# Kernel tuning notes

Hardware: AMD Instinct MI355X
Metric: run time of the kernel (lower is better)

## Reference

```python
import jax, jax.numpy as jnp
import numpy as np

NUM_GRAPHS = 512

def setup_inputs() -> dict:
    key = jax.random.key(0)
    ks = jax.random.split(key, 6)
    N, E, D = 100000, 1600000, 128
    x = jax.random.normal(ks[0], (N, D), dtype=jnp.float32)
    edge_index = jax.random.randint(ks[1], (2, E), 0, N, dtype=jnp.int64)
    batch = jnp.sort(jax.random.randint(ks[2], (N,), 0, NUM_GRAPHS, dtype=jnp.int64))
    scale = 1.0 / np.sqrt(D)
    Ws = jax.random.normal(ks[3], (4, D, D), dtype=jnp.float32) * scale
    bs = jnp.zeros((4, D), dtype=jnp.float32)
    Wl = jax.random.normal(ks[4], (D, 1), dtype=jnp.float32) * scale
    bl = jnp.zeros((1,), dtype=jnp.float32)
    return {"x": x, "edge_index": edge_index, "batch": batch,
            "Ws": Ws, "bs": bs, "Wl": Wl, "bl": bl}

def reference(x, edge_index, batch, Ws, bs, Wl, bl):
    N = x.shape[0]
    loops = jnp.arange(N, dtype=edge_index.dtype)
    # GCNConv: add self-loops, symmetric normalization D^{-1/2} A D^{-1/2}
    row = jnp.concatenate([edge_index[0], loops])  # source nodes
    col = jnp.concatenate([edge_index[1], loops])  # target nodes
    deg = jax.ops.segment_sum(jnp.ones_like(col, dtype=x.dtype), col, num_segments=N)
    dinv = jnp.where(deg > 0, jax.lax.rsqrt(jnp.maximum(deg, 1.0)), 0.0)
    norm = dinv[row] * dinv[col]  # [E+N]
    h = x
    for i in range(Ws.shape[0]):
        h = h @ Ws[i]                                   # [N, D]
        msg = h[row] * norm[:, None]                    # gather + scale, [E+N, D]
        h = jax.ops.segment_sum(msg, col, num_segments=N) + bs[i]
        h = jax.nn.relu(h)                              # dropout is identity in eval
    # global_mean_pool over graphs
    sums = jax.ops.segment_sum(h, batch, num_segments=NUM_GRAPHS)
    cnt = jax.ops.segment_sum(jnp.ones((N,), h.dtype), batch, num_segments=NUM_GRAPHS)
    pooled = sums / jnp.maximum(cnt, 1.0)[:, None]      # [G, D]
    return pooled @ Wl + bl                             # [G, 1]
```

## Files before the change

kernel.cpp:

```cpp
#include <hip/hip_runtime.h>


constexpr int D = 128;
constexpr int NGRAPH = 512;
constexpr int CHUNK = 4096;
constexpr int BSH = 9;
constexpr int OP = 136;

typedef __attribute__((ext_vector_type(8))) short bf16x8;
typedef __attribute__((ext_vector_type(4))) float f32x4;

__device__ __forceinline__ float bf2f(unsigned short b) {
    return __uint_as_float(((unsigned int)b) << 16);
}
__device__ __forceinline__ unsigned short f2bf(float f) {
    unsigned int u = __float_as_uint(f);
    u += 0x7FFFu + ((u >> 16) & 1u);
    return (unsigned short)(u >> 16);
}

__global__ __launch_bounds__(256) void setup_all(
        const float4* __restrict__ x4, ushort4* __restrict__ hb, int n4, int CB,
        const float* __restrict__ W, unsigned short* __restrict__ Wt,
        const int* __restrict__ ec, int E, int* __restrict__ bucketCnt) {
    __shared__ int h[256];
    const int t = threadIdx.x;
    const int b = blockIdx.x;
    if (b < CB) {
        int i = b * 256 + t;
        if (i < n4) {
            float4 v = x4[i];
            ushort4 o;
            o.x = f2bf(v.x); o.y = f2bf(v.y); o.z = f2bf(v.z); o.w = f2bf(v.w);
            hb[i] = o;
        }
    } else if (b < CB + 256) {
        int idx = (b - CB) * 256 + t;
        int i = idx >> 14;
        int rem = idx & 16383;
        int k = rem >> 7, c = rem & 127;
        Wt[(i << 14) + c * 128 + k] = f2bf(W[idx]);
    } else {
        h[t] = 0;
        __syncthreads();
        const int e0 = (b - CB - 256) * CHUNK;
        const int cnt = min(CHUNK, E - e0);
        for (int i = t; i < cnt; i += 256) atomicAdd(&h[ec[e0 + i] >> BSH], 1);
        __syncthreads();
        if (h[t]) atomicAdd(&bucketCnt[t], h[t]);
    }
}

__global__ __launch_bounds__(256) void bucket_scan(const int* __restrict__ bucketCnt,
                                                   int* __restrict__ bucketBase,
                                                   int* __restrict__ globCursor) {
    __shared__ int s[256];
    const int t = threadIdx.x;
    int v = bucketCnt[t];
    s[t] = v; __syncthreads();
    for (int off = 1; off < 256; off <<= 1) {
        int x = (t >= off) ? s[t - off] : 0;
        __syncthreads();
        s[t] += x;
        __syncthreads();
    }
    int excl = s[t] - v;
    bucketBase[t] = excl;
    globCursor[t] = excl;
}

__global__ __launch_bounds__(256) void scatter_pairs(const int* __restrict__ er,
                                                     const int* __restrict__ ec, int E,
                                                     int* __restrict__ globCursor,
                                                     int2* __restrict__ pairs) {
    __shared__ int h[256], lbase[256], cur[256], segd[256], s[256];
    __shared__ int2 stage[CHUNK];
    const int t = threadIdx.x;
    const int e0 = blockIdx.x * CHUNK;
    const int cnt = min(CHUNK, E - e0);

    h[t] = 0;
    __syncthreads();
    for (int i = t; i < cnt; i += 256) atomicAdd(&h[ec[e0 + i] >> BSH], 1);
    __syncthreads();
    int v = h[t];
    s[t] = v; __syncthreads();
    for (int off = 1; off < 256; off <<= 1) {
        int x = (t >= off) ? s[t - off] : 0;
        __syncthreads();
        s[t] += x;
        __syncthreads();
    }
    lbase[t] = s[t] - v;
    cur[t] = s[t] - v;
    segd[t] = atomicAdd(&globCursor[t], v) - lbase[t];
    __syncthreads();
    for (int i = t; i < cnt; i += 256) {
        int c = ec[e0 + i];
        int b = c >> BSH;
        int p = atomicAdd(&cur[b], 1);
        stage[p] = make_int2(er[e0 + i], c);
    }
    __syncthreads();
    for (int i = t; i < cnt; i += 256) {
        int2 pr = stage[i];
        int b = pr.y >> BSH;
        pairs[segd[b] + i] = pr;
    }
}

__global__ __launch_bounds__(256) void fill_csr(const int2* __restrict__ pairs,
                                                const int* __restrict__ bucketBase,
                                                const int* __restrict__ bucketCnt,
                                                int N, int E, int NBUCK,
                                                int* __restrict__ rowptr,
                                                float* __restrict__ dinv,
                                                int* __restrict__ srcs) {
    __shared__ int hist[512], lofs[512], s[256];
    const int t = threadIdx.x;
    const int b = blockIdx.x;
    const int c0 = b << BSH;
    const int base = bucketBase[b];
    const int cnt = bucketCnt[b];
    const int2* pp = pairs + base;

    hist[t] = 0; hist[t + 256] = 0;
    __syncthreads();
    for (int i = t; i < cnt; i += 256) atomicAdd(&hist[pp[i].y - c0], 1);
    __syncthreads();
    int a0 = hist[2 * t], a1 = hist[2 * t + 1];
    s[t] = a0 + a1; __syncthreads();
    for (int off = 1; off < 256; off <<= 1) {
        int x = (t >= off) ? s[t - off] : 0;
        __syncthreads();
        s[t] += x;
        __syncthreads();
    }
    int excl = s[t] - (a0 + a1);
    lofs[2 * t] = excl;
    lofs[2 * t + 1] = excl + a0;
    __syncthreads();
    const int nn = min(512, N - c0);
    for (int i = t; i < nn; i += 256) {
        rowptr[c0 + i] = base + lofs[i];
        dinv[c0 + i] = rsqrtf((float)hist[i] + 1.0f);
    }
    if (b == NBUCK - 1 && t == 0) rowptr[N] = E;
    __syncthreads();
    for (int i = t; i < cnt; i += 256) {
        int2 pr = pp[i];
        int p = atomicAdd(&lofs[pr.y - c0], 1);
        srcs[base + p] = pr.x;
    }
}

__global__ __launch_bounds__(64, 4) void layer_fused(
        const int* __restrict__ rowptr, const int* __restrict__ srcs,
        const float* __restrict__ dinv, const unsigned short* __restrict__ H,
        const unsigned short* __restrict__ Wt, const float* __restrict__ bias,
        unsigned short* __restrict__ Hn, float* __restrict__ dots,
        const float* __restrict__ Wl, int N, int preScaled, int writeDots) {
    __shared__ __align__(16) unsigned short U[32 * OP];
    const int lane = threadIdx.x;
    const int row16 = lane & 15;
    const int quad = lane >> 4;
    const int r0 = blockIdx.x * 32;
    const bf16x8* H8 = (const bf16x8*)H;

    {
        const int gl = row16;
        const int rb = quad * 8;
        for (int sstep = 0; sstep < 8; ++sstep) {
            const int rt = rb + sstep;
            const int row = r0 + rt;
            float acc[8] = {0.f, 0.f, 0.f, 0.f, 0.f, 0.f, 0.f, 0.f};
            float sn = 0.f;
            if (row < N) {
                sn = dinv[row];
                int j = rowptr[row];
                const int end = rowptr[row + 1];
                bf16x8 hv = H8[(size_t)row * 16 + gl];
                const float sf = preScaled ? 1.f : sn;
#pragma unroll
                for (int k = 0; k < 8; ++k) acc[k] = sf * bf2f((unsigned short)hv[k]);
                if (preScaled) {
                    for (; j + 8 <= end; j += 8) {
                        int r[8]; bf16x8 h[8];
#pragma unroll
                        for (int t = 0; t < 8; ++t) r[t] = srcs[j + t];
#pragma unroll
                        for (int t = 0; t < 8; ++t) h[t] = H8[(size_t)r[t] * 16 + gl];
#pragma unroll
                        for (int t = 0; t < 8; ++t)
#pragma unroll
                            for (int k = 0; k < 8; ++k)
                                acc[k] += bf2f((unsigned short)h[t][k]);
                    }
                    for (; j < end; ++j) {
                        bf16x8 h0 = H8[(size_t)srcs[j] * 16 + gl];
#pragma unroll
                        for (int k = 0; k < 8; ++k)
                            acc[k] += bf2f((unsigned short)h0[k]);
                    }
                } else {
                    for (; j + 8 <= end; j += 8) {
                        int r[8]; float sc[8]; bf16x8 h[8];
#pragma unroll
                        for (int t = 0; t < 8; ++t) r[t] = srcs[j + t];
#pragma unroll
                        for (int t = 0; t < 8; ++t) sc[t] = dinv[r[t]];
#pragma unroll
                        for (int t = 0; t < 8; ++t) h[t] = H8[(size_t)r[t] * 16 + gl];
#pragma unroll
                        for (int t = 0; t < 8; ++t)
#pragma unroll
                            for (int k = 0; k < 8; ++k)
                                acc[k] += sc[t] * bf2f((unsigned short)h[t][k]);
                    }
                    for (; j < end; ++j) {
                        int r00 = srcs[j];
                        float s0 = dinv[r00];
                        bf16x8 h0 = H8[(size_t)r00 * 16 + gl];
#pragma unroll
                        for (int k = 0; k < 8; ++k)
                            acc[k] += s0 * bf2f((unsigned short)h0[k]);
                    }
                }
            }
            bf16x8 o;
#pragma unroll
            for (int k = 0; k < 8; ++k) o[k] = (short)f2bf(sn * acc[k]);
            *(bf16x8*)(U + rt * 128 + ((gl ^ (rt & 15)) << 3)) = o;
        }
    }
    __syncthreads();

    bf16x8 a0[4], a1[4];
#pragma unroll
    for (int kc = 0; kc < 4; ++kc) {
        const int ph = (kc * 4 + quad) ^ row16;
        a0[kc] = *(const bf16x8*)(U + row16 * 128 + ph * 8);
        a1[kc] = *(const bf16x8*)(U + (16 + row16) * 128 + ph * 8);
    }
    __syncthreads();

    float dvA[4], dvB[4];
    if (!writeDots) {
#pragma unroll
        for (int i = 0; i < 4; ++i) {
            int ra = r0 + quad * 4 + i;
            int rbg = ra + 16;
            dvA[i] = (ra < N) ? dinv[ra] : 0.f;
            dvB[i] = (rbg < N) ? dinv[rbg] : 0.f;
        }
    }

    float rd0[4] = {0.f, 0.f, 0.f, 0.f}, rd1[4] = {0.f, 0.f, 0.f, 0.f};
#pragma unroll
    for (int ct = 0; ct < 8; ++ct) {
        const int col = ct * 16 + row16;
        const bf16x8* wc = (const bf16x8*)(Wt + (size_t)col * 128);
        f32x4 acc0 = {0.f, 0.f, 0.f, 0.f}, acc1 = {0.f, 0.f, 0.f, 0.f};
#pragma unroll
        for (int kc = 0; kc < 4; ++kc) {
            const bf16x8 wf = wc[kc * 4 + quad];
            acc0 = __builtin_amdgcn_mfma_f32_16x16x32_bf16(a0[kc], wf, acc0, 0, 0, 0);
            acc1 = __builtin_amdgcn_mfma_f32_16x16x32_bf16(a1[kc], wf, acc1, 0, 0, 0);
        }
        const float bv = bias[col];
        if (writeDots) {
            const float wl = Wl[col];
#pragma unroll
            for (int i = 0; i < 4; ++i) {
                rd0[i] += fmaxf(acc0[i] + bv, 0.f) * wl;
                rd1[i] += fmaxf(acc1[i] + bv, 0.f) * wl;
            }
        } else {
#pragma unroll
            for (int i = 0; i < 4; ++i) {
                U[(quad * 4 + i) * OP + col] = f2bf(dvA[i] * fmaxf(acc0[i] + bv, 0.f));
                U[(16 + quad * 4 + i) * OP + col] = f2bf(dvB[i] * fmaxf(acc1[i] + bv, 0.f));
            }
        }
    }

    if (writeDots) {
#pragma unroll
        for (int m = 1; m < 16; m <<= 1)
#pragma unroll
            for (int i = 0; i < 4; ++i) {
                rd0[i] += __shfl_xor(rd0[i], m, 64);
                rd1[i] += __shfl_xor(rd1[i], m, 64);
            }
        if (row16 == 0) {
#pragma unroll
            for (int i = 0; i < 4; ++i) {
                dots[r0 + quad * 4 + i] = rd0[i];
                dots[r0 + 16 + quad * 4 + i] = rd1[i];
            }
        }
    } else {
        __syncthreads();
#pragma unroll
        for (int i = 0; i < 8; ++i) {
            int idx = i * 64 + lane;
            int row = idx >> 4, c8 = idx & 15;
            bf16x8 v = *(const bf16x8*)(U + row * OP + c8 * 8);
            *(bf16x8*)(Hn + (size_t)(r0 + row) * 128 + c8 * 8) = v;
        }
    }
}

__global__ __launch_bounds__(256) void pool_graphs(const float* __restrict__ dots,
                                                   const int* __restrict__ batch, int N,
                                                   const float* __restrict__ bl,
                                                   float* __restrict__ out) {
    __shared__ int bounds[2];
    __shared__ float red[4];
    const int g = blockIdx.x;
    const int t = threadIdx.x;
    if (t < 2) {
        int key = g + t;
        int lo = 0, hi = N;
        while (lo < hi) {
            int mid = (lo + hi) >> 1;
            if (batch[mid] < key) lo = mid + 1; else hi = mid;
        }
        bounds[t] = lo;
    }
    __syncthreads();
    const int lo = bounds[0], hi = bounds[1];
    float s = 0.f;
    for (int i = lo + t; i < hi; i += 256) s += dots[i];
#pragma unroll
    for (int off = 32; off > 0; off >>= 1) s += __shfl_down(s, off, 64);
    if ((t & 63) == 0) red[t >> 6] = s;
    __syncthreads();
    if (t == 0) {
        float tot = red[0] + red[1] + red[2] + red[3];
        int cnt = hi - lo;
        out[g] = tot / (float)(cnt > 0 ? cnt : 1) + bl[0];
    }
}

extern "C" void kernel_launch(void* const* d_in, const int* in_sizes, int n_in,
                              void* d_out, int out_size, void* d_ws, size_t ws_size,
                              hipStream_t stream) {
    const float* x     = (const float*)d_in[0];
    const int*   eidx  = (const int*)d_in[1];
    const int*   batch = (const int*)d_in[2];
    const float* Ws    = (const float*)d_in[3];
    const float* bs    = (const float*)d_in[4];
    const float* Wl    = (const float*)d_in[5];
    const float* bl    = (const float*)d_in[6];
    (void)n_in; (void)out_size;

    const int N = in_sizes[0] / D;
    const int E = in_sizes[1] / 2;
    const int* er = eidx;
    const int* ec = eidx + E;
    const int NBUCK = (N + 511) >> BSH;
    const int NCHUNK = (E + CHUNK - 1) / CHUNK;

    const int Npad = (N + 127) & ~127;
    const size_t hBytes = (size_t)Npad * D * sizeof(unsigned short);
    auto al = [](size_t v) { return (v + 255) & ~(size_t)255; };
    char* base = (char*)d_ws;
    size_t off = 0;

    unsigned short* Hb0 = (unsigned short*)base; off = al(hBytes);
    int* bucketCnt  = (int*)(base + off);
    int* globCursor = bucketCnt + 256;
    off = al(off + 512 * sizeof(int));
    int*   bucketBase = (int*)(base + off);  off = al(off + 256 * sizeof(int));
    float* dinv   = (float*)(base + off);    off = al(off + (size_t)Npad * sizeof(float));
    float* dots   = (float*)(base + off);    off = al(off + (size_t)Npad * sizeof(float));
    int*   rowptr = (int*)(base + off);      off = al(off + (size_t)(Npad + 64) * sizeof(int));
    int*   srcs   = (int*)(base + off);      off = al(off + (size_t)E * sizeof(int));
    unsigned short* Wt = (unsigned short*)(base + off);   off = al(off + 4 * 128 * 128 * sizeof(unsigned short));

    const bool twoBuf = ws_size >= off + hBytes;
    unsigned short* Hb1 = twoBuf ? (unsigned short*)(base + off)
                                 : (unsigned short*)d_in[0];
    int2* pairs = (int2*)Hb1;
    unsigned short* hb[2] = { Hb0, Hb1 };

    hipMemsetAsync(bucketCnt, 0, 256 * sizeof(int), stream);
    const int n4 = N * D / 4;
    const int CB = (n4 + 255) / 256;
    setup_all<<<CB + 256 + NCHUNK, 256, 0, stream>>>((const float4*)x, (ushort4*)Hb0,
                                                     n4, CB, Ws, Wt, ec, E, bucketCnt);

    bucket_scan<<<1, 256, 0, stream>>>(bucketCnt, bucketBase, globCursor);
    scatter_pairs<<<NCHUNK, 256, 0, stream>>>(er, ec, E, globCursor, pairs);
    fill_csr<<<NBUCK, 256, 0, stream>>>(pairs, bucketBase, bucketCnt, N, E, NBUCK,
                                        rowptr, dinv, srcs);

    for (int i = 0; i < 4; ++i) {
        const unsigned short* Hc = hb[i & 1];
        unsigned short* Hn = hb[(i + 1) & 1];
        layer_fused<<<Npad / 32, 64, 0, stream>>>(rowptr, srcs, dinv, Hc,
                                                  Wt + (size_t)i * D * D,
                                                  bs + (size_t)i * D, Hn, dots, Wl,
                                                  N, (i > 0) ? 1 : 0,
                                                  (i == 3) ? 1 : 0);
    }

    pool_graphs<<<NGRAPH, 256, 0, stream>>>(dots, batch, N, bl, (float*)d_out);
}
```

Measured before the change: 477.2 us.

## Pre-scale input features in CSR build and shrink layer tile to 16 rows

The first layer's D^-1/2 source scaling now happens inside fill_csr, which rescales the bf16 input rows in place. That removes the non-prescaled path and the per-edge dinv gathers from layer_fused. The layer kernel processes 16 rows per block instead of 32, giving twice as many blocks and a higher occupancy bound. The gather loop uses vector index loads with next-batch prefetch, masked tails instead of a scalar remainder loop, and packed f32x2 accumulation. In exchange, the MFMA weight loads are amortised over fewer rows, and masked lanes issue redundant gathers of the self row.

```diff
diff --git a/kernel.cpp b/kernel.cpp
--- a/kernel.cpp
+++ b/kernel.cpp
@@ -9,6 +9,8 @@
 
 typedef __attribute__((ext_vector_type(8))) short bf16x8;
 typedef __attribute__((ext_vector_type(4))) float f32x4;
+typedef __attribute__((ext_vector_type(2))) float f32x2;
+typedef int i32x4u __attribute__((ext_vector_type(4), aligned(4)));
 
 __device__ __forceinline__ float bf2f(unsigned short b) {
     return __uint_as_float(((unsigned int)b) << 16);
@@ -17,6 +19,12 @@
     unsigned int u = __float_as_uint(f);
     u += 0x7FFFu + ((u >> 16) & 1u);
     return (unsigned short)(u >> 16);
+}
+__device__ __forceinline__ f32x2 unpk(unsigned int d) {
+    f32x2 r;
+    r.x = __uint_as_float(d << 16);
+    r.y = __uint_as_float(d & 0xFFFF0000u);
+    return r;
 }
 
 __global__ __launch_bounds__(256) void setup_all(
@@ -115,7 +123,8 @@
                                                 int N, int E, int NBUCK,
                                                 int* __restrict__ rowptr,
                                                 float* __restrict__ dinv,
-                                                int* __restrict__ srcs) {
+                                                int* __restrict__ srcs,
+                                                unsigned short* __restrict__ Hb0) {
     __shared__ int hist[512], lofs[512], s[256];
     const int t = threadIdx.x;
     const int b = blockIdx.x;
@@ -152,135 +161,126 @@
         int p = atomicAdd(&lofs[pr.y - c0], 1);
         srcs[base + p] = pr.x;
     }
-}
-
-__global__ __launch_bounds__(64, 4) void layer_fused(
+    unsigned int* Hrow = (unsigned int*)Hb0 + (size_t)c0 * 64;
+    for (int i = t; i < nn * 64; i += 256) {
+        int r = i >> 6;
+        float dv = rsqrtf((float)hist[r] + 1.0f);
+        unsigned int v = Hrow[i];
+        unsigned short lo = f2bf(bf2f((unsigned short)(v & 0xFFFFu)) * dv);
+        unsigned short hi = f2bf(bf2f((unsigned short)(v >> 16)) * dv);
+        Hrow[i] = ((unsigned int)hi << 16) | lo;
+    }
+}
+
+__global__ __launch_bounds__(64, 8) void layer_fused(
         const int* __restrict__ rowptr, const int* __restrict__ srcs,
         const float* __restrict__ dinv, const unsigned short* __restrict__ H,
         const unsigned short* __restrict__ Wt, const float* __restrict__ bias,
         unsigned short* __restrict__ Hn, float* __restrict__ dots,
-        const float* __restrict__ Wl, int N, int preScaled, int writeDots) {
-    __shared__ __align__(16) unsigned short U[32 * OP];
+        const float* __restrict__ Wl, int N, int writeDots) {
+    __shared__ __align__(16) unsigned short U[16 * OP];
     const int lane = threadIdx.x;
     const int row16 = lane & 15;
     const int quad = lane >> 4;
-    const int r0 = blockIdx.x * 32;
+    const int r0 = blockIdx.x * 16;
     const bf16x8* H8 = (const bf16x8*)H;
-
-    {
-        const int gl = row16;
-        const int rb = quad * 8;
-        for (int sstep = 0; sstep < 8; ++sstep) {
-            const int rt = rb + sstep;
-            const int row = r0 + rt;
-            float acc[8] = {0.f, 0.f, 0.f, 0.f, 0.f, 0.f, 0.f, 0.f};
-            float sn = 0.f;
-            if (row < N) {
-                sn = dinv[row];
-                int j = rowptr[row];
-                const int end = rowptr[row + 1];
-                bf16x8 hv = H8[(size_t)row * 16 + gl];
-                const float sf = preScaled ? 1.f : sn;
-#pragma unroll
-                for (int k = 0; k < 8; ++k) acc[k] = sf * bf2f((unsigned short)hv[k]);
-                if (preScaled) {
-                    for (; j + 8 <= end; j += 8) {
-                        int r[8]; bf16x8 h[8];
-#pragma unroll
-                        for (int t = 0; t < 8; ++t) r[t] = srcs[j + t];
-#pragma unroll
-                        for (int t = 0; t < 8; ++t) h[t] = H8[(size_t)r[t] * 16 + gl];
-#pragma unroll
-                        for (int t = 0; t < 8; ++t)
-#pragma unroll
-                            for (int k = 0; k < 8; ++k)
-                                acc[k] += bf2f((unsigned short)h[t][k]);
-                    }
-                    for (; j < end; ++j) {
-                        bf16x8 h0 = H8[(size_t)srcs[j] * 16 + gl];
-#pragma unroll
-                        for (int k = 0; k < 8; ++k)
-                            acc[k] += bf2f((unsigned short)h0[k]);
-                    }
-                } else {
-                    for (; j + 8 <= end; j += 8) {
-                        int r[8]; float sc[8]; bf16x8 h[8];
-#pragma unroll
-                        for (int t = 0; t < 8; ++t) r[t] = srcs[j + t];
-#pragma unroll
-                        for (int t = 0; t < 8; ++t) sc[t] = dinv[r[t]];
-#pragma unroll
-                        for (int t = 0; t < 8; ++t) h[t] = H8[(size_t)r[t] * 16 + gl];
-#pragma unroll
-                        for (int t = 0; t < 8; ++t)
-#pragma unroll
-                            for (int k = 0; k < 8; ++k)
-                                acc[k] += sc[t] * bf2f((unsigned short)h[t][k]);
-                    }
-                    for (; j < end; ++j) {
-                        int r00 = srcs[j];
-                        float s0 = dinv[r00];
-                        bf16x8 h0 = H8[(size_t)r00 * 16 + gl];
-#pragma unroll
-                        for (int k = 0; k < 8; ++k)
-                            acc[k] += s0 * bf2f((unsigned short)h0[k]);
-                    }
+    const int gl = row16;
+
+    for (int sstep = 0; sstep < 4; ++sstep) {
+        const int rt = quad * 4 + sstep;
+        const int row = r0 + rt;
+        f32x2 acc[4] = {{0.f, 0.f}, {0.f, 0.f}, {0.f, 0.f}, {0.f, 0.f}};
+        float sn = 0.f;
+        if (row < N) {
+            sn = dinv[row];
+            int j = rowptr[row];
+            const int end = rowptr[row + 1];
+            {
+                union { bf16x8 v; unsigned int d[4]; } sv;
+                sv.v = H8[(size_t)row * 16 + gl];
+#pragma unroll
+                for (int i = 0; i < 4; ++i) acc[i] = unpk(sv.d[i]);
+            }
+            const int nb = (end - j + 7) >> 3;
+            i32x4u ia, ib;
+            if (nb > 0) {
+                const i32x4u* sp = (const i32x4u*)(srcs + j);
+                ia = sp[0]; ib = sp[1];
+            }
+            for (int b = 0; b < nb; ++b) {
+                const int jb = j + b * 8;
+                int r[8]; float w[8];
+#pragma unroll
+                for (int t = 0; t < 8; ++t) {
+                    int idx = (t < 4) ? ia[t] : ib[t - 4];
+                    bool val = (jb + t) < end;
+                    r[t] = val ? idx : row;
+                    w[t] = val ? 1.f : 0.f;
+                }
+                bf16x8 h[8];
+#pragma unroll
+                for (int t = 0; t < 8; ++t) h[t] = H8[(size_t)r[t] * 16 + gl];
+                if (b + 1 < nb) {
+                    const i32x4u* sp = (const i32x4u*)(srcs + jb + 8);
+                    ia = sp[0]; ib = sp[1];
+                }
+#pragma unroll
+                for (int t = 0; t < 8; ++t) {
+                    union { bf16x8 v; unsigned int d[4]; } cv;
+                    cv.v = h[t];
+                    f32x2 w2 = {w[t], w[t]};
+#pragma unroll
+                    for (int i = 0; i < 4; ++i) acc[i] += unpk(cv.d[i]) * w2;
                 }
             }
-            bf16x8 o;
-#pragma unroll
-            for (int k = 0; k < 8; ++k) o[k] = (short)f2bf(sn * acc[k]);
-            *(bf16x8*)(U + rt * 128 + ((gl ^ (rt & 15)) << 3)) = o;
-        }
-    }
-    __syncthreads();
-
-    bf16x8 a0[4], a1[4];
+        }
+        bf16x8 o;
+#pragma unroll
+        for (int i = 0; i < 4; ++i) {
+            o[2 * i]     = (short)f2bf(sn * acc[i].x);
+            o[2 * i + 1] = (short)f2bf(sn * acc[i].y);
+        }
+        *(bf16x8*)(U + rt * 128 + ((gl ^ rt) << 3)) = o;
+    }
+    __syncthreads();
+
+    bf16x8 a0[4];
 #pragma unroll
     for (int kc = 0; kc < 4; ++kc) {
         const int ph = (kc * 4 + quad) ^ row16;
         a0[kc] = *(const bf16x8*)(U + row16 * 128 + ph * 8);
-        a1[kc] = *(const bf16x8*)(U + (16 + row16) * 128 + ph * 8);
-    }
-    __syncthreads();
-
-    float dvA[4], dvB[4];
+    }
+    __syncthreads();
+
+    float dv[4];
     if (!writeDots) {
 #pragma unroll
         for (int i = 0; i < 4; ++i) {
             int ra = r0 + quad * 4 + i;
-            int rbg = ra + 16;
-            dvA[i] = (ra < N) ? dinv[ra] : 0.f;
-            dvB[i] = (rbg < N) ? dinv[rbg] : 0.f;
-        }
-    }
-
-    float rd0[4] = {0.f, 0.f, 0.f, 0.f}, rd1[4] = {0.f, 0.f, 0.f, 0.f};
+            dv[i] = (ra < N) ? dinv[ra] : 0.f;
+        }
+    }
+
+    float rd[4] = {0.f, 0.f, 0.f, 0.f};
 #pragma unroll
     for (int ct = 0; ct < 8; ++ct) {
         const int col = ct * 16 + row16;
         const bf16x8* wc = (const bf16x8*)(Wt + (size_t)col * 128);
-        f32x4 acc0 = {0.f, 0.f, 0.f, 0.f}, acc1 = {0.f, 0.f, 0.f, 0.f};
+        f32x4 acc0 = {0.f, 0.f, 0.f, 0.f};
 #pragma unroll
         for (int kc = 0; kc < 4; ++kc) {
             const bf16x8 wf = wc[kc * 4 + quad];
             acc0 = __builtin_amdgcn_mfma_f32_16x16x32_bf16(a0[kc], wf, acc0, 0, 0, 0);
-            acc1 = __builtin_amdgcn_mfma_f32_16x16x32_bf16(a1[kc], wf, acc1, 0, 0, 0);
         }
         const float bv = bias[col];
         if (writeDots) {
             const float wl = Wl[col];
 #pragma unroll
-            for (int i = 0; i < 4; ++i) {
-                rd0[i] += fmaxf(acc0[i] + bv, 0.f) * wl;
-                rd1[i] += fmaxf(acc1[i] + bv, 0.f) * wl;
-            }
+            for (int i = 0; i < 4; ++i) rd[i] += fmaxf(acc0[i] + bv, 0.f) * wl;
         } else {
 #pragma unroll
-            for (int i = 0; i < 4; ++i) {
-                U[(quad * 4 + i) * OP + col] = f2bf(dvA[i] * fmaxf(acc0[i] + bv, 0.f));
-                U[(16 + quad * 4 + i) * OP + col] = f2bf(dvB[i] * fmaxf(acc1[i] + bv, 0.f));
-            }
+            for (int i = 0; i < 4; ++i)
+                U[(quad * 4 + i) * OP + col] = f2bf(dv[i] * fmaxf(acc0[i] + bv, 0.f));
         }
     }
 
@@ -288,21 +288,15 @@
 #pragma unroll
         for (int m = 1; m < 16; m <<= 1)
 #pragma unroll
-            for (int i = 0; i < 4; ++i) {
-                rd0[i] += __shfl_xor(rd0[i], m, 64);
-                rd1[i] += __shfl_xor(rd1[i], m, 64);
-            }
+            for (int i = 0; i < 4; ++i) rd[i] += __shfl_xor(rd[i], m, 64);
         if (row16 == 0) {
 #pragma unroll
-            for (int i = 0; i < 4; ++i) {
-                dots[r0 + quad * 4 + i] = rd0[i];
-                dots[r0 + 16 + quad * 4 + i] = rd1[i];
-            }
+            for (int i = 0; i < 4; ++i) dots[r0 + quad * 4 + i] = rd[i];
         }
     } else {
         __syncthreads();
 #pragma unroll
-        for (int i = 0; i < 8; ++i) {
+        for (int i = 0; i < 4; ++i) {
             int idx = i * 64 + lane;
             int row = idx >> 4, c8 = idx & 15;
             bf16x8 v = *(const bf16x8*)(U + row * OP + c8 * 8);
@@ -376,7 +370,7 @@
     float* dinv   = (float*)(base + off);    off = al(off + (size_t)Npad * sizeof(float));
     float* dots   = (float*)(base + off);    off = al(off + (size_t)Npad * sizeof(float));
     int*   rowptr = (int*)(base + off);      off = al(off + (size_t)(Npad + 64) * sizeof(int));
-    int*   srcs   = (int*)(base + off);      off = al(off + (size_t)E * sizeof(int));
+    int*   srcs   = (int*)(base + off);      off = al(off + (size_t)E * sizeof(int) + 64);
     unsigned short* Wt = (unsigned short*)(base + off);   off = al(off + 4 * 128 * 128 * sizeof(unsigned short));
 
     const bool twoBuf = ws_size >= off + hBytes;
@@ -394,16 +388,15 @@
     bucket_scan<<<1, 256, 0, stream>>>(bucketCnt, bucketBase, globCursor);
     scatter_pairs<<<NCHUNK, 256, 0, stream>>>(er, ec, E, globCursor, pairs);
     fill_csr<<<NBUCK, 256, 0, stream>>>(pairs, bucketBase, bucketCnt, N, E, NBUCK,
-                                        rowptr, dinv, srcs);
+                                        rowptr, dinv, srcs, Hb0);
 
     for (int i = 0; i < 4; ++i) {
         const unsigned short* Hc = hb[i & 1];
         unsigned short* Hn = hb[(i + 1) & 1];
-        layer_fused<<<Npad / 32, 64, 0, stream>>>(rowptr, srcs, dinv, Hc,
+        layer_fused<<<Npad / 16, 64, 0, stream>>>(rowptr, srcs, dinv, Hc,
                                                   Wt + (size_t)i * D * D,
                                                   bs + (size_t)i * D, Hn, dots, Wl,
-                                                  N, (i > 0) ? 1 : 0,
-                                                  (i == 3) ? 1 : 0);
+                                                  N, (i == 3) ? 1 : 0);
     }
 
     pool_graphs<<<NGRAPH, 256, 0, stream>>>(dots, batch, N, bl, (float*)d_out);
```

Result: slower. 616.5 us (+29.2%).
